# Kernel optimization log

Measured on AMD Instinct MI355X. Metric: run time of the kernel, lower is better.

## Reference

```python
import jax, jax.numpy as jnp
import numpy as np
import math

B, N, DIM, H, DH = 2, 2048, 768, 12, 64
NUM_BUCKETS, MAX_DIST = 32, 128


def _rel_pos_bucket(n):
    # causal bucketing as in T5RelativePositionBias._relative_position_bucket
    rel = jnp.arange(n)[None, :] - jnp.arange(n)[:, None]          # k_pos - q_pos
    neg = jnp.maximum(-rel, 0)                                     # n = max(-rel, 0)
    max_exact = NUM_BUCKETS // 2
    is_small = neg < max_exact
    val_large = max_exact + (
        jnp.log(jnp.maximum(neg, 1).astype(jnp.float32) / max_exact)
        / math.log(MAX_DIST / max_exact) * (NUM_BUCKETS - max_exact)
    ).astype(jnp.int32)
    val_large = jnp.minimum(val_large, NUM_BUCKETS - 1)
    return jnp.where(is_small, neg, val_large)                     # [n, n] int32


def setup_inputs() -> dict:
    key = jax.random.key(0)
    ks = jax.random.split(key, 6)
    s = DIM ** -0.5
    x = jax.random.normal(ks[0], (B, N, DIM), jnp.float32)
    mask = jnp.ones((B, N), dtype=bool)
    Wq = jax.random.normal(ks[1], (DIM, H * DH), jnp.float32) * s
    Wk = jax.random.normal(ks[2], (DIM, H * DH), jnp.float32) * s
    Wv = jax.random.normal(ks[3], (DIM, H * DH), jnp.float32) * s
    Wo = jax.random.normal(ks[4], (H * DH, DIM), jnp.float32) * s
    rel_emb = jax.random.normal(ks[5], (NUM_BUCKETS, H), jnp.float32) * 0.02
    return {"x": x, "mask": mask, "Wq": Wq, "Wk": Wk, "Wv": Wv, "Wo": Wo, "rel_emb": rel_emb}


def reference(x, mask, Wq, Wk, Wv, Wo, rel_emb):
    b, n, _ = x.shape
    scale = DH ** -0.5
    # projections -> [b, h, n, d]
    q = (x @ Wq).reshape(b, n, H, DH).transpose(0, 2, 1, 3) * scale
    k = (x @ Wk).reshape(b, n, H, DH).transpose(0, 2, 1, 3)
    v = (x @ Wv).reshape(b, n, H, DH).transpose(0, 2, 1, 3)
    sim = jnp.einsum('bhid,bhjd->bhij', q, k)                      # [b, h, n, n]
    # relative position bias, also scaled by dim_head**-0.5
    bias = rel_emb[_rel_pos_bucket(n)]                             # [n, n, h]
    sim = sim + jnp.transpose(bias, (2, 0, 1))[None] * scale
    mask_value = -jnp.finfo(sim.dtype).max
    # key/query padding mask: ~mask[:, None, :, None] masks rows (query dim)
    sim = jnp.where(mask[:, None, :, None], sim, mask_value)
    causal = jnp.triu(jnp.ones((n, n), dtype=bool), 1)
    sim = jnp.where(causal[None, None], mask_value, sim)
    attn = jax.nn.softmax(sim, axis=-1)
    out = jnp.einsum('bhij,bhjd->bhid', attn, v)                   # [b, h, n, d]
    out = out.transpose(0, 2, 1, 3).reshape(b, n, H * DH)
    return out @ Wo
```

## Files before the change

### kernel.cpp

```cpp
#include <hip/hip_runtime.h>
#include <math.h>

#define NSEQ 2048
#define HDIM 768
#define NHEAD 12
#define DHEAD 64
#define CHUNK 6
#define NJOBS 102
#define EXP_C1 1.44269504f
#define EXP_C0 -17.3123405f

typedef __attribute__((ext_vector_type(8))) short short8;
typedef __attribute__((ext_vector_type(4))) float f32x4;

static __device__ __forceinline__ unsigned short f2bf(float x) {
    unsigned int u = __float_as_uint(x);
    unsigned int r = (u + 0x7fffu + ((u >> 16) & 1u)) >> 16;
    return (unsigned short)r;
}
static __device__ __forceinline__ float bf2f(unsigned short u) {
    return __uint_as_float(((unsigned int)u) << 16);
}

#define GLD_LDS16(g, l)                                                  \
    __builtin_amdgcn_global_load_lds(                                    \
        (const __attribute__((address_space(1))) void*)(g),              \
        (__attribute__((address_space(3))) void*)(l), 16, 0, 0)

__global__ __launch_bounds__(256) void prep(const float* __restrict__ X,
                                            const float* __restrict__ Wq,
                                            const float* __restrict__ Wk,
                                            const float* __restrict__ Wv,
                                            const float* __restrict__ Wo,
                                            const float* __restrict__ relemb,
                                            unsigned short* __restrict__ Xb,
                                            unsigned short* __restrict__ Wt,
                                            unsigned short* __restrict__ rbg) {
    __shared__ float tbuf[32][33];
    const int z = blockIdx.x;
    if (z < 2304) {
        const int wsel = z / 576, tt = z % 576;
        const int n0 = (tt % 24) * 32, k0 = (tt / 24) * 32;
        const float* W = (wsel == 0) ? Wq : (wsel == 1) ? Wk : (wsel == 2) ? Wv : Wo;
        const float scale = (wsel == 0) ? 0.125f : 1.0f;
        unsigned short* dst = Wt + (size_t)wsel * HDIM * HDIM;
        const int r = threadIdx.x >> 3, c4 = threadIdx.x & 7;
        float4 v = *(const float4*)(W + (size_t)(k0 + r) * HDIM + n0 + c4 * 4);
        tbuf[c4 * 4 + 0][r] = v.x;
        tbuf[c4 * 4 + 1][r] = v.y;
        tbuf[c4 * 4 + 2][r] = v.z;
        tbuf[c4 * 4 + 3][r] = v.w;
        __syncthreads();
        ushort4 o;
        o.x = f2bf(tbuf[r][c4 * 4 + 0] * scale);
        o.y = f2bf(tbuf[r][c4 * 4 + 1] * scale);
        o.z = f2bf(tbuf[r][c4 * 4 + 2] * scale);
        o.w = f2bf(tbuf[r][c4 * 4 + 3] * scale);
        *(ushort4*)(dst + (size_t)(n0 + r) * HDIM + k0 + c4 * 4) = o;
    } else if (z < 2688) {
        int base = (z - 2304) * 2048 + threadIdx.x;
#pragma unroll
        for (int u = 0; u < 8; u++) {
            int f = base + u * 256;
            float4 v = ((const float4*)X)[f];
            ushort4 o;
            o.x = f2bf(v.x); o.y = f2bf(v.y); o.z = f2bf(v.z); o.w = f2bf(v.w);
            ((ushort4*)Xb)[f] = o;
        }
    } else {
        int idx = (z - 2688) * 256 + threadIdx.x;
        int h = idx >> 11;
        int d = idx & (NSEQ - 1);
        int bucket;
        if (d < 16) {
            bucket = d;
        } else {
            float v = logf((float)d * (1.0f / 16.0f)) * (16.0f / logf(8.0f));
            bucket = 16 + (int)v;
            if (bucket > 31) bucket = 31;
        }
        rbg[h * NSEQ + d] = f2bf(relemb[bucket * NHEAD + h] * 0.125f);
    }
}

template <int MODE>
__global__ __launch_bounds__(256) void gemm_bt(const unsigned short* __restrict__ A,
                                               const unsigned short* __restrict__ Bt,
                                               void* __restrict__ Cout) {
    __shared__ unsigned short As[128 * 32];
    __shared__ unsigned short Bs[128 * 32];

    const int tid = threadIdx.x;
    const int w = tid >> 6, lane = tid & 63;
    const int ln = lane & 15, qd = lane >> 4;
    const int wm = w >> 1, wn = w & 1;
    const int mat = blockIdx.x / (HDIM / 128);
    const int n0 = (blockIdx.x % (HDIM / 128)) * 128;
    const int m0 = blockIdx.y * 128;
    const unsigned short* Bm = Bt + (size_t)mat * HDIM * HDIM;

    const int srow = w * 32 + (lane >> 2);
    const int scol = (lane & 3) * 8;
    const unsigned short* agp = A + (size_t)(m0 + srow) * HDIM + scol;
    const unsigned short* bgp = Bm + (size_t)(n0 + srow) * HDIM + scol;
    unsigned short* al = As + (w * 32) * 32;
    unsigned short* bl = Bs + (w * 32) * 32;

    f32x4 acc[4][4];
#pragma unroll
    for (int i = 0; i < 4; i++)
#pragma unroll
        for (int j = 0; j < 4; j++) acc[i][j] = (f32x4){0.f, 0.f, 0.f, 0.f};

    for (int k0 = 0; k0 < HDIM; k0 += 32) {
        __syncthreads();
        GLD_LDS16(agp + k0, al);
        GLD_LDS16(agp + 16 * HDIM + k0, al + 16 * 32);
        GLD_LDS16(bgp + k0, bl);
        GLD_LDS16(bgp + 16 * HDIM + k0, bl + 16 * 32);
        __syncthreads();

        short8 af[4], bf[4];
#pragma unroll
        for (int mt = 0; mt < 4; mt++)
            af[mt] = *(const short8*)&As[(wm * 64 + mt * 16 + ln) * 32 + qd * 8];
#pragma unroll
        for (int nt = 0; nt < 4; nt++)
            bf[nt] = *(const short8*)&Bs[(wn * 64 + nt * 16 + ln) * 32 + qd * 8];
#pragma unroll
        for (int mt = 0; mt < 4; mt++)
#pragma unroll
            for (int nt = 0; nt < 4; nt++)
                acc[mt][nt] = __builtin_amdgcn_mfma_f32_16x16x32_bf16(
                    af[mt], bf[nt], acc[mt][nt], 0, 0, 0);
    }

    if (MODE == 0) {
        float* C = (float*)Cout;
#pragma unroll
        for (int mt = 0; mt < 4; mt++)
#pragma unroll
            for (int r = 0; r < 4; r++) {
                int m = m0 + wm * 64 + mt * 16 + qd * 4 + r;
#pragma unroll
                for (int nt = 0; nt < 4; nt++) {
                    int n = n0 + wn * 64 + nt * 16 + ln;
                    C[(size_t)m * HDIM + n] = acc[mt][nt][r];
                }
            }
    } else {
        const size_t QKVE = (size_t)2 * NHEAD * NSEQ * DHEAD;
        unsigned short* dstm = (unsigned short*)Cout + (size_t)mat * QKVE;
#pragma unroll
        for (int mt = 0; mt < 4; mt++)
#pragma unroll
            for (int r = 0; r < 4; r++) {
                int m = m0 + wm * 64 + mt * 16 + qd * 4 + r;
                int b = m >> 11, tok = m & (NSEQ - 1);
#pragma unroll
                for (int nt = 0; nt < 4; nt++) {
                    int col = n0 + wn * 64 + nt * 16 + ln;
                    int h = col >> 6, dh = col & 63;
                    dstm[((size_t)(b * NHEAD + h) * NSEQ + tok) * DHEAD + dh] =
                        f2bf(acc[mt][nt][r]);
                }
            }
    }
}

__global__ __launch_bounds__(256) void vtrans(const unsigned short* __restrict__ Vn,
                                              unsigned short* __restrict__ Vt) {
    __shared__ unsigned short Ls[64 * 66];
    const int tid = threadIdx.x;
    const int tok0 = blockIdx.x * 64;
    const size_t bh = blockIdx.y;
    const unsigned short* src = Vn + (bh * NSEQ + tok0) * DHEAD;
    unsigned short* dst = Vt + bh * DHEAD * NSEQ + tok0;

    const int rr = tid >> 3, cc = (tid & 7) * 8;
#pragma unroll
    for (int u = 0; u < 2; u++)
        *(short8*)&Ls[(u * 32 + rr) * 66 + cc] =
            *(const short8*)(src + (size_t)(u * 32 + rr) * DHEAD + cc);
    __syncthreads();
#pragma unroll
    for (int u = 0; u < 2; u++) {
        int dhr = u * 32 + rr;
        short8 v;
#pragma unroll
        for (int e = 0; e < 8; e++) v[e] = Ls[(cc + e) * 66 + dhr];
        *(short8*)(dst + (size_t)dhr * NSEQ + cc) = v;
    }
}

__global__ __launch_bounds__(256) void attn_mfma(const unsigned short* __restrict__ Q,
                                                 const unsigned short* __restrict__ K,
                                                 const unsigned short* __restrict__ Vt_g,
                                                 const unsigned short* __restrict__ rbg,
                                                 unsigned short* __restrict__ Of,
                                                 float* __restrict__ Pl) {
    __shared__ __align__(16) unsigned short Ks[64 * 72];
    __shared__ __align__(16) unsigned short Vt[64 * 72];
    __shared__ __align__(16) unsigned short Ps[4 * 16 * 72];
    __shared__ __align__(16) unsigned short rbs[64 + NSEQ];

    const int tid = threadIdx.x;
    const int w = tid >> 6;
    const int lane = tid & 63;
    const int ln = lane & 15;
    const int qd = lane >> 4;
    const int job = blockIdx.x;
    const int h = blockIdx.y;
    const int b = blockIdx.z;

    int q = 0, cb = 0;
    for (;;) {
        int c = (q + CHUNK) / CHUNK;
        if (job < cb + c) break;
        cb += c;
        q++;
    }
    const int c = (q + CHUNK) / CHUNK;
    const int jd = job - cb;
    const int nt = q + 1;
    const int t0 = nt * jd / c, t1 = nt * (jd + 1) / c;
    const int i0 = q * 64;

    const int bhl = b * NHEAD + h;
    const size_t bh = (size_t)bhl;
    const unsigned short* Kb = K + bh * NSEQ * DHEAD;
    const unsigned short* Vg = Vt_g + bh * DHEAD * NSEQ;

    const unsigned short NEG = f2bf(-1e30f);
    if (tid < 8) {
        short8 n8;
#pragma unroll
        for (int e = 0; e < 8; e++) n8[e] = (short)NEG;
        *(short8*)&rbs[tid * 8] = n8;
    }
    *(short8*)&rbs[64 + tid * 8] = ((const short8*)(rbg + h * NSEQ))[tid];

    const unsigned short* qrow = Q + (bh * NSEQ + i0 + w * 16 + ln) * DHEAD;
    const short8 qf0 = *(const short8*)(qrow + qd * 8);
    const short8 qf1 = *(const short8*)(qrow + 32 + qd * 8);

    short8 ones;
#pragma unroll
    for (int e = 0; e < 8; e++) ones[e] = (short)0x3F80;

    f32x4 o[4] = {{0.f, 0.f, 0.f, 0.f}, {0.f, 0.f, 0.f, 0.f},
                  {0.f, 0.f, 0.f, 0.f}, {0.f, 0.f, 0.f, 0.f}};
    f32x4 o4 = {0.f, 0.f, 0.f, 0.f};

    const int irow_base = i0 + w * 16 + qd * 4;
    const int bq = irow_base + 64 - ln;
    unsigned short* Pw = Ps + w * 16 * 72;

    const int sr = tid >> 3;
    const int sc = (tid & 7) * 8;
    short8 kp[2], vp[2];
    {
        const int jb = t0 * 64;
#pragma unroll
        for (int u = 0; u < 2; u++) {
            kp[u] = *(const short8*)(Kb + (size_t)(jb + u * 32 + sr) * DHEAD + sc);
            vp[u] = *(const short8*)(Vg + (size_t)(u * 32 + sr) * NSEQ + jb + sc);
        }
    }

    for (int t = t0; t < t1; t++) {
        const int jt = t * 64;
        __syncthreads();
#pragma unroll
        for (int u = 0; u < 2; u++) {
            *(short8*)&Ks[(u * 32 + sr) * 72 + sc] = kp[u];
            *(short8*)&Vt[(u * 32 + sr) * 72 + sc] = vp[u];
        }
        __syncthreads();
        if (t + 1 < t1) {
            const int jn = jt + 64;
#pragma unroll
            for (int u = 0; u < 2; u++) {
                kp[u] = *(const short8*)(Kb + (size_t)(jn + u * 32 + sr) * DHEAD + sc);
                vp[u] = *(const short8*)(Vg + (size_t)(u * 32 + sr) * NSEQ + jn + sc);
            }
        }

        f32x4 s[4] = {{0.f, 0.f, 0.f, 0.f}, {0.f, 0.f, 0.f, 0.f},
                      {0.f, 0.f, 0.f, 0.f}, {0.f, 0.f, 0.f, 0.f}};
#pragma unroll
        for (int cc = 0; cc < 4; cc++) {
            short8 b0 = *(const short8*)&Ks[(cc * 16 + ln) * 72 + qd * 8];
            short8 b1 = *(const short8*)&Ks[(cc * 16 + ln) * 72 + 32 + qd * 8];
            s[cc] = __builtin_amdgcn_mfma_f32_16x16x32_bf16(qf0, b0, s[cc], 0, 0, 0);
            s[cc] = __builtin_amdgcn_mfma_f32_16x16x32_bf16(qf1, b1, s[cc], 0, 0, 0);
        }

#pragma unroll
        for (int cc = 0; cc < 4; cc++) {
            const int ib = bq - jt - cc * 16;
#pragma unroll
            for (int r = 0; r < 4; r++) {
                float sv = s[cc][r] + bf2f(rbs[ib + r]);
                float p = __builtin_amdgcn_exp2f(__fmaf_rn(sv, EXP_C1, EXP_C0));
                Pw[(qd * 4 + r) * 72 + cc * 16 + ln] = f2bf(p);
            }
        }

        short8 pa0 = *(const short8*)(Pw + ln * 72 + qd * 8);
        short8 pa1 = *(const short8*)(Pw + ln * 72 + 32 + qd * 8);

#pragma unroll
        for (int cc = 0; cc < 4; cc++) {
            short8 vb0 = *(const short8*)&Vt[(cc * 16 + ln) * 72 + qd * 8];
            short8 vb1 = *(const short8*)&Vt[(cc * 16 + ln) * 72 + 32 + qd * 8];
            o[cc] = __builtin_amdgcn_mfma_f32_16x16x32_bf16(pa0, vb0, o[cc], 0, 0, 0);
            o[cc] = __builtin_amdgcn_mfma_f32_16x16x32_bf16(pa1, vb1, o[cc], 0, 0, 0);
        }
        o4 = __builtin_amdgcn_mfma_f32_16x16x32_bf16(pa0, ones, o4, 0, 0, 0);
        o4 = __builtin_amdgcn_mfma_f32_16x16x32_bf16(pa1, ones, o4, 0, 0, 0);
    }

    const size_t gc = (size_t)bhl * NJOBS + job;
    const int rowl = w * 16 + qd * 4;
    unsigned short* po = Of + (gc * 64 + rowl) * 64 + ln;
#pragma unroll
    for (int r = 0; r < 4; r++) {
        float inv = 1.0f / o4[r];
#pragma unroll
        for (int cc = 0; cc < 4; cc++)
            po[(size_t)r * 64 + cc * 16] = f2bf(o[cc][r] * inv);
    }
    if (ln == 0) {
#pragma unroll
        for (int r = 0; r < 4; r++) Pl[gc * 64 + rowl + r] = o4[r];
    }
}

__global__ __launch_bounds__(256) void attn_merge(const unsigned short* __restrict__ Of,
                                                  const float* __restrict__ Pl,
                                                  unsigned short* __restrict__ AO) {
    const int tid = threadIdx.x;
    const int row_g = blockIdx.x * 4 + (tid >> 6);
    const int dh = tid & 63;
    const int bhl = row_g >> 11;
    const int tok = row_g & (NSEQ - 1);
    const int b = bhl / NHEAD, h = bhl % NHEAD;
    const int q = tok >> 6;

    int cb = 0;
    for (int qq = 0; qq < q; qq++) cb += (qq + CHUNK) / CHUNK;
    const int c = (q + CHUNK) / CHUNK;
    const int rowl = tok & 63;

    float acc = 0.f, W = 0.f;
    for (int i = 0; i < c; i++) {
        size_t gc = (size_t)bhl * NJOBS + cb + i;
        float l = Pl[gc * 64 + rowl];
        acc += l * bf2f(Of[(gc * 64 + rowl) * 64 + dh]);
        W += l;
    }
    AO[((size_t)(b * NSEQ) + tok) * HDIM + h * DHEAD + dh] = f2bf(acc / W);
}

extern "C" void kernel_launch(void* const* d_in, const int* in_sizes, int n_in,
                              void* d_out, int out_size, void* d_ws, size_t ws_size,
                              hipStream_t stream) {
    const float* x      = (const float*)d_in[0];
    const float* Wq     = (const float*)d_in[2];
    const float* Wk     = (const float*)d_in[3];
    const float* Wv     = (const float*)d_in[4];
    const float* Wo     = (const float*)d_in[5];
    const float* relemb = (const float*)d_in[6];
    float* out = (float*)d_out;

    const size_t QKV = (size_t)2 * NHEAD * NSEQ * DHEAD;
    const size_t NCHUNK = (size_t)24 * NJOBS;
    unsigned short* q   = (unsigned short*)d_ws;
    unsigned short* k   = q + QKV;
    unsigned short* v   = k + QKV;
    unsigned short* vT  = v + QKV;
    unsigned short* aob = vT + QKV;
    unsigned short* xb  = aob + QKV;
    unsigned short* wt  = xb + QKV;
    unsigned short* rbg = wt + (size_t)4 * HDIM * HDIM;
    unsigned short* Of  = rbg + (size_t)NHEAD * NSEQ;
    float* Pl = (float*)(Of + NCHUNK * 64 * 64);

    prep<<<2784, 256, 0, stream>>>(x, Wq, Wk, Wv, Wo, relemb, xb, wt, rbg);

    gemm_bt<1><<<dim3(3 * HDIM / 128, (2 * NSEQ) / 128), 256, 0, stream>>>(xb, wt, q);

    vtrans<<<dim3(NSEQ / 64, 2 * NHEAD), 256, 0, stream>>>(v, vT);

    attn_mfma<<<dim3(NJOBS, NHEAD, 2), 256, 0, stream>>>(q, k, vT, rbg, Of, Pl);

    attn_merge<<<(2 * NHEAD * NSEQ) / 4, 256, 0, stream>>>(Of, Pl, aob);

    gemm_bt<0><<<dim3(HDIM / 128, (2 * NSEQ) / 128), 256, 0, stream>>>(
        aob, wt + (size_t)3 * HDIM * HDIM, out);
}
```

Measured before the change: 198.2 us.

## Write single-chunk attention rows directly and shrink merge and weight-prep grids

Query blocks 0-5 are covered by a single key chunk, so the attention kernel now writes their normalized output straight into the final AO buffer. The merge kernel is launched only for tokens 384 and beyond, and its chunk offset comes from a closed-form expression instead of a loop. The weight transpose in prep now uses 64x64 tiles with four rows per thread, cutting its block count. The result depends on the chunk-to-job mapping matching the closed-form offset and on the first CHUNK jobs being exactly the single-chunk query blocks.

```diff
diff --git a/kernel.cpp b/kernel.cpp
--- a/kernel.cpp
+++ b/kernel.cpp
@@ -36,29 +36,38 @@
                                             unsigned short* __restrict__ Xb,
                                             unsigned short* __restrict__ Wt,
                                             unsigned short* __restrict__ rbg) {
-    __shared__ float tbuf[32][33];
+    __shared__ float tb[64][65];
     const int z = blockIdx.x;
-    if (z < 2304) {
-        const int wsel = z / 576, tt = z % 576;
-        const int n0 = (tt % 24) * 32, k0 = (tt / 24) * 32;
+    if (z < 576) {
+        const int wsel = z / 144, tt = z % 144;
+        const int n0 = (tt % 12) * 64, k0 = (tt / 12) * 64;
         const float* W = (wsel == 0) ? Wq : (wsel == 1) ? Wk : (wsel == 2) ? Wv : Wo;
         const float scale = (wsel == 0) ? 0.125f : 1.0f;
         unsigned short* dst = Wt + (size_t)wsel * HDIM * HDIM;
-        const int r = threadIdx.x >> 3, c4 = threadIdx.x & 7;
-        float4 v = *(const float4*)(W + (size_t)(k0 + r) * HDIM + n0 + c4 * 4);
-        tbuf[c4 * 4 + 0][r] = v.x;
-        tbuf[c4 * 4 + 1][r] = v.y;
-        tbuf[c4 * 4 + 2][r] = v.z;
-        tbuf[c4 * 4 + 3][r] = v.w;
+        const int r = threadIdx.x >> 4;
+        const int c4 = (threadIdx.x & 15) * 4;
+#pragma unroll
+        for (int i = 0; i < 4; i++) {
+            int row = i * 16 + r;
+            float4 v = *(const float4*)(W + (size_t)(k0 + row) * HDIM + n0 + c4);
+            tb[c4 + 0][row] = v.x * scale;
+            tb[c4 + 1][row] = v.y * scale;
+            tb[c4 + 2][row] = v.z * scale;
+            tb[c4 + 3][row] = v.w * scale;
+        }
         __syncthreads();
-        ushort4 o;
-        o.x = f2bf(tbuf[r][c4 * 4 + 0] * scale);
-        o.y = f2bf(tbuf[r][c4 * 4 + 1] * scale);
-        o.z = f2bf(tbuf[r][c4 * 4 + 2] * scale);
-        o.w = f2bf(tbuf[r][c4 * 4 + 3] * scale);
-        *(ushort4*)(dst + (size_t)(n0 + r) * HDIM + k0 + c4 * 4) = o;
-    } else if (z < 2688) {
-        int base = (z - 2304) * 2048 + threadIdx.x;
+#pragma unroll
+        for (int i = 0; i < 4; i++) {
+            int row = i * 16 + r;
+            ushort4 o;
+            o.x = f2bf(tb[row][c4 + 0]);
+            o.y = f2bf(tb[row][c4 + 1]);
+            o.z = f2bf(tb[row][c4 + 2]);
+            o.w = f2bf(tb[row][c4 + 3]);
+            *(ushort4*)(dst + (size_t)(n0 + row) * HDIM + k0 + c4) = o;
+        }
+    } else if (z < 960) {
+        int base = (z - 576) * 2048 + threadIdx.x;
 #pragma unroll
         for (int u = 0; u < 8; u++) {
             int f = base + u * 256;
@@ -68,7 +77,7 @@
             ((ushort4*)Xb)[f] = o;
         }
     } else {
-        int idx = (z - 2688) * 256 + threadIdx.x;
+        int idx = (z - 960) * 256 + threadIdx.x;
         int h = idx >> 11;
         int d = idx & (NSEQ - 1);
         int bucket;
@@ -197,6 +206,7 @@
                                                  const unsigned short* __restrict__ K,
                                                  const unsigned short* __restrict__ Vt_g,
                                                  const unsigned short* __restrict__ rbg,
+                                                 unsigned short* __restrict__ AO,
                                                  unsigned short* __restrict__ Of,
                                                  float* __restrict__ Pl) {
     __shared__ __align__(16) unsigned short Ks[64 * 72];
@@ -321,19 +331,31 @@
         o4 = __builtin_amdgcn_mfma_f32_16x16x32_bf16(pa1, ones, o4, 0, 0, 0);
     }
 
-    const size_t gc = (size_t)bhl * NJOBS + job;
-    const int rowl = w * 16 + qd * 4;
-    unsigned short* po = Of + (gc * 64 + rowl) * 64 + ln;
-#pragma unroll
-    for (int r = 0; r < 4; r++) {
-        float inv = 1.0f / o4[r];
-#pragma unroll
-        for (int cc = 0; cc < 4; cc++)
-            po[(size_t)r * 64 + cc * 16] = f2bf(o[cc][r] * inv);
-    }
-    if (ln == 0) {
-#pragma unroll
-        for (int r = 0; r < 4; r++) Pl[gc * 64 + rowl + r] = o4[r];
+    if (job < CHUNK) {
+        unsigned short* aop =
+            AO + ((size_t)(b * NSEQ) + i0 + w * 16 + qd * 4) * HDIM + h * DHEAD + ln;
+#pragma unroll
+        for (int r = 0; r < 4; r++) {
+            float inv = 1.0f / o4[r];
+#pragma unroll
+            for (int cc = 0; cc < 4; cc++)
+                aop[(size_t)r * HDIM + cc * 16] = f2bf(o[cc][r] * inv);
+        }
+    } else {
+        const size_t gc = (size_t)bhl * NJOBS + job;
+        const int rowl = w * 16 + qd * 4;
+        unsigned short* po = Of + (gc * 64 + rowl) * 64 + ln;
+#pragma unroll
+        for (int r = 0; r < 4; r++) {
+            float inv = 1.0f / o4[r];
+#pragma unroll
+            for (int cc = 0; cc < 4; cc++)
+                po[(size_t)r * 64 + cc * 16] = f2bf(o[cc][r] * inv);
+        }
+        if (ln == 0) {
+#pragma unroll
+            for (int r = 0; r < 4; r++) Pl[gc * 64 + rowl + r] = o4[r];
+        }
     }
 }
 
@@ -343,14 +365,14 @@
     const int tid = threadIdx.x;
     const int row_g = blockIdx.x * 4 + (tid >> 6);
     const int dh = tid & 63;
-    const int bhl = row_g >> 11;
-    const int tok = row_g & (NSEQ - 1);
+    const int bhl = row_g / (NSEQ - 384);
+    const int tok = 384 + row_g % (NSEQ - 384);
     const int b = bhl / NHEAD, h = bhl % NHEAD;
     const int q = tok >> 6;
 
-    int cb = 0;
-    for (int qq = 0; qq < q; qq++) cb += (qq + CHUNK) / CHUNK;
-    const int c = (q + CHUNK) / CHUNK;
+    const int g = q / CHUNK, rr = q % CHUNK;
+    const int cb = 3 * g * (g + 1) + rr * (g + 1);
+    const int c = g + 1;
     const int rowl = tok & 63;
 
     float acc = 0.f, W = 0.f;
@@ -387,15 +409,15 @@
     unsigned short* Of  = rbg + (size_t)NHEAD * NSEQ;
     float* Pl = (float*)(Of + NCHUNK * 64 * 64);
 
-    prep<<<2784, 256, 0, stream>>>(x, Wq, Wk, Wv, Wo, relemb, xb, wt, rbg);
+    prep<<<1056, 256, 0, stream>>>(x, Wq, Wk, Wv, Wo, relemb, xb, wt, rbg);
 
     gemm_bt<1><<<dim3(3 * HDIM / 128, (2 * NSEQ) / 128), 256, 0, stream>>>(xb, wt, q);
 
     vtrans<<<dim3(NSEQ / 64, 2 * NHEAD), 256, 0, stream>>>(v, vT);
 
-    attn_mfma<<<dim3(NJOBS, NHEAD, 2), 256, 0, stream>>>(q, k, vT, rbg, Of, Pl);
-
-    attn_merge<<<(2 * NHEAD * NSEQ) / 4, 256, 0, stream>>>(Of, Pl, aob);
+    attn_mfma<<<dim3(NJOBS, NHEAD, 2), 256, 0, stream>>>(q, k, vT, rbg, aob, Of, Pl);
+
+    attn_merge<<<(24 * (NSEQ - 384)) / 4, 256, 0, stream>>>(Of, Pl, aob);
 
     gemm_bt<0><<<dim3(HDIM / 128, (2 * NSEQ) / 128), 256, 0, stream>>>(
         aob, wt + (size_t)3 * HDIM * HDIM, out);
```

New measurement: 193.8 us. -2.2%, faster.
